# Performance work log

Hardware: AMD Instinct MI355X
Metric: run time of the kernel (lower is better)

## Reference

```python
import jax, jax.numpy as jnp
import numpy as np

T_STEPS, B, NMUL = 365, 20000, 4
NEARZERO = 1e-06

_BOUNDS = {
    'parBETA': (1.0, 6.0), 'parFC': (50.0, 1000.0), 'parK0': (0.05, 0.9),
    'parK1': (0.01, 0.5), 'parK2': (0.001, 0.2), 'parLP': (0.2, 1.0),
    'parPERC': (0.0, 10.0), 'parUZL': (0.0, 100.0), 'parTT': (-2.5, 2.5),
    'parCFMAX': (0.5, 10.0), 'parCFR': (0.0, 0.1), 'parCWH': (0.0, 0.2),
    'parBETAET': (0.3, 5.0), 'parC': (0.0, 1.0),
}


def setup_inputs() -> dict:
    key = jax.random.key(0)
    kf, kt, kp, *pkeys = jax.random.split(key, 3 + len(_BOUNDS))
    # forcing (T, B, 3): [prcp (mm/d), tmean (degC), pet (mm/d)]
    prcp = jax.random.uniform(kf, (T_STEPS, B), jnp.float32) * 10.0
    tmean = jax.random.normal(kt, (T_STEPS, B), jnp.float32) * 10.0
    pet = jax.random.uniform(kp, (T_STEPS, B), jnp.float32) * 5.0
    inp = {'forcing': jnp.stack([prcp, tmean, pet], axis=-1)}
    for k_rng, (name, (lo, hi)) in zip(pkeys, _BOUNDS.items()):
        inp[name] = jax.random.uniform(k_rng, (B, NMUL), jnp.float32, lo, hi)
    return inp


def _hbv_scan(forcing, parTT, parCFMAX, parCFR, parCWH, parFC, parBETA, parLP,
              parBETAET, parC, parPERC, parK0, parK1, parK2, parUZL):
    eps = NEARZERO
    nmul = parTT.shape[-1]
    n_grid = forcing.shape[1]
    # expand forcing to (T, B, nmul)
    Pm = jnp.broadcast_to(forcing[:, :, 0:1], forcing.shape[:2] + (nmul,))
    Tm = jnp.broadcast_to(forcing[:, :, 1:2], forcing.shape[:2] + (nmul,))
    PETm = jnp.broadcast_to(forcing[:, :, 2:3], forcing.shape[:2] + (nmul,))

    snow0 = jnp.full((n_grid, nmul), eps, forcing.dtype)
    zeros = jnp.zeros((n_grid, nmul), forcing.dtype)

    def step(carry, x):
        snow, melt, sm, suz, slz = carry
        p, t_val, pet = x
        temp_diff = t_val - parTT
        is_rain = temp_diff > 0.0
        rain = jnp.where(is_rain, p, 0.0)
        snow_input = jnp.where(is_rain, 0.0, p)
        snow1 = snow + snow_input
        pot_melt = parCFMAX * jnp.maximum(temp_diff, 0.0)
        melt_amount = jnp.minimum(pot_melt, snow1)
        snow2 = snow1 - melt_amount
        melt1 = melt + melt_amount
        pot_refreeze = parCFR * parCFMAX * jnp.maximum(-temp_diff, 0.0)
        refreeze = jnp.minimum(pot_refreeze, melt1)
        snow_out = snow2 + refreeze
        melt2 = melt1 - refreeze
        tosoil = jnp.maximum(melt2 - parCWH * snow_out, 0.0)
        melt_out = melt2 - tosoil
        soil_wet = jnp.clip(jnp.power(jnp.maximum(sm / parFC, eps), parBETA), 0.0, 1.0)
        recharge = (rain + tosoil) * soil_wet
        sm1 = sm + rain + tosoil - recharge
        excess = jnp.maximum(sm1 - parFC, 0.0)
        sm2 = sm1 - excess
        ef1 = jnp.clip(sm2 / (parLP * parFC), 0.0, 1.0)
        evapfactor = jnp.clip(jnp.power(jnp.maximum(ef1, eps), parBETAET), 0.0, 1.0)
        etact = jnp.minimum(pet * evapfactor, sm2)
        sm_ae = jnp.maximum(sm2 - etact, eps)
        sm_ratio = jnp.minimum(sm_ae / parFC, 1.0)
        capillary = jnp.minimum(slz, parC * slz * (1.0 - sm_ratio))
        sm_out = jnp.maximum(sm_ae + capillary, eps)
        slz_ac = jnp.maximum(slz - capillary, eps)
        suz1 = suz + recharge + excess
        perc_flux = jnp.minimum(suz1, parPERC)
        suz2 = suz1 - perc_flux
        slz1 = slz_ac + perc_flux
        q0 = parK0 * jnp.maximum(suz2 - parUZL, 0.0)
        suz3 = suz2 - q0
        q1 = parK1 * suz3
        suz_out = suz3 - q1
        q2 = parK2 * slz1
        slz_out = slz1 - q2
        q = q0 + q1 + q2
        return (snow_out, melt_out, sm_out, suz_out, slz_out), q

    _, Qsim = jax.lax.scan(step, (snow0, zeros, zeros, zeros, zeros), (Pm, Tm, PETm))
    return Qsim  # (T, B, nmul)


def reference(forcing, parTT, parCFMAX, parCFR, parCWH, parFC, parBETA, parLP,
              parBETAET, parC, parPERC, parK0, parK1, parK2, parUZL):
    Qsim = _hbv_scan(forcing, parTT, parCFMAX, parCFR, parCWH, parFC, parBETA,
                     parLP, parBETAET, parC, parPERC, parK0, parK1, parK2, parUZL)
    Qsim_avg = Qsim.mean(axis=-1)  # 'streamflow' (T, B)
    return (Qsim_avg, Qsim)
```

## Files before the change

### kernel.cpp

```cpp
#include <hip/hip_runtime.h>

#define TSTEPS 365
#define BGRID  20000
#define NMUL   4
#define NEARZERO 1e-6f
#define C    8
#define V    2
#define NCH  (TSTEPS / C)
#define TAIL (TSTEPS - NCH * C)

struct F3 { float p, t, pet; };

__device__ __forceinline__ float pair_swap(float x) {
    int a = __builtin_amdgcn_update_dpp(0, __float_as_int(x),
                                        0xB1 , 0xF, 0xF, true);
    return __int_as_float(a);
}

__device__ __forceinline__ float fast_log2(float x) { return __builtin_amdgcn_logf(x); }
__device__ __forceinline__ float fast_exp2(float x) { return __builtin_amdgcn_exp2f(x); }

#define LOAD_CHUNK(BUF, N)                                                  \
    _Pragma("unroll")                                                       \
    for (int j_ = 0; j_ < (N); ++j_) { BUF[j_] = *fp; fp += BGRID; }

#define STORE_CHUNK(QS, N)                                                  \
    _Pragma("unroll")                                                       \
    for (int j_ = 0; j_ < (N); ++j_) {                                      \
        qq[0] = QS[j_][0]; qq[2] = QS[j_][1]; qq += BGRID * NMUL;           \
        const float h_ = QS[j_][0] + QS[j_][1];                             \
        *qa = (h_ + pair_swap(h_)) * 0.25f; qa += BGRID;                    \
    }

#define COMPUTE_CHUNK(BUF, QO, N)                                           \
    _Pragma("unroll")                                                       \
    for (int j_ = 0; j_ < (N); ++j_) { step(BUF[j_], QO[j_]); }

__global__ __launch_bounds__(64) __attribute__((amdgpu_waves_per_eu(1, 2)))
void hbv_fwd(
    const float* __restrict__ forcing,
    const float* __restrict__ pBETA,  const float* __restrict__ pFC,
    const float* __restrict__ pK0,    const float* __restrict__ pK1,
    const float* __restrict__ pK2,    const float* __restrict__ pLP,
    const float* __restrict__ pPERC,  const float* __restrict__ pUZL,
    const float* __restrict__ pTT,    const float* __restrict__ pCFMAX,
    const float* __restrict__ pCFR,   const float* __restrict__ pCWH,
    const float* __restrict__ pBETAET,const float* __restrict__ pC,
    float* __restrict__ out_avg,
    float* __restrict__ out_q)
{
    const int tid = blockIdx.x * 64 + threadIdx.x;
    const int b  = tid >> 1;
    const int c0 = (b << 2) + (tid & 1);

    float parBETA[V], parFC[V], parK0[V], parK1[V], parK2[V], parPERC[V],
          parUZL[V], parTT[V], parCFMAX[V], parCWH[V], parBETAET[V], parC[V],
          refreeze_coef[V], inv_FC[V], inv_LPFC[V];
#pragma unroll
    for (int v = 0; v < V; ++v) {
        const int c = c0 + 2 * v;
        parBETA[v]   = pBETA[c];   parFC[v]   = pFC[c];
        parK0[v]     = pK0[c];     parK1[v]   = pK1[c];
        parK2[v]     = pK2[c];     parPERC[v] = pPERC[c];
        parUZL[v]    = pUZL[c];    parTT[v]   = pTT[c];
        parCFMAX[v]  = pCFMAX[c];  parCWH[v]  = pCWH[c];
        parBETAET[v] = pBETAET[c]; parC[v]    = pC[c];
        refreeze_coef[v] = pCFR[c] * parCFMAX[v];
        inv_FC[v]   = 1.0f / parFC[v];
        inv_LPFC[v] = 1.0f / (pLP[c] * parFC[v]);
    }

    float snow[V], melt[V], sm[V], suz[V], slz[V];
#pragma unroll
    for (int v = 0; v < V; ++v) {
        snow[v] = NEARZERO; melt[v] = 0.0f; sm[v] = 0.0f; suz[v] = 0.0f; slz[v] = 0.0f;
    }

    const F3* __restrict__ fp = (const F3*)forcing + b;
    float* __restrict__ qq = out_q + c0;
    float* __restrict__ qa = out_avg + b;

    auto step = [&](const F3 fv, float (&qo)[V]) {
#pragma unroll
        for (int v = 0; v < V; ++v) {
            const float temp_diff = fv.t - parTT[v];
            const bool  is_rain = temp_diff > 0.0f;
            const float rain       = is_rain ? fv.p : 0.0f;
            const float snow_input = is_rain ? 0.0f : fv.p;
            float snow1 = snow[v] + snow_input;
            const float pot_melt = parCFMAX[v] * fmaxf(temp_diff, 0.0f);
            const float melt_amount = fminf(pot_melt, snow1);
            snow1 -= melt_amount;
            float melt1 = melt[v] + melt_amount;
            const float pot_refreeze = refreeze_coef[v] * fmaxf(-temp_diff, 0.0f);
            const float refreeze = fminf(pot_refreeze, melt1);
            snow[v] = snow1 + refreeze;
            melt1 -= refreeze;
            const float tosoil = fmaxf(melt1 - parCWH[v] * snow[v], 0.0f);
            melt[v] = melt1 - tosoil;

            const float x1 = fmaxf(sm[v] * inv_FC[v], NEARZERO);
            const float soil_wet = fminf(fast_exp2(parBETA[v] * fast_log2(x1)), 1.0f);
            const float rt = rain + tosoil;
            const float recharge = rt * soil_wet;
            float sm1 = sm[v] + rt - recharge;
            const float excess = fmaxf(sm1 - parFC[v], 0.0f);
            sm1 -= excess;
            const float ef1 = fminf(sm1 * inv_LPFC[v], 1.0f);
            const float x2 = fmaxf(ef1, NEARZERO);
            const float evapfactor = fminf(fast_exp2(parBETAET[v] * fast_log2(x2)), 1.0f);
            const float etact = fminf(fv.pet * evapfactor, sm1);
            const float sm_ae = fmaxf(sm1 - etact, NEARZERO);
            const float sm_ratio = fminf(sm_ae * inv_FC[v], 1.0f);
            const float capillary = fminf(slz[v], parC[v] * slz[v] * (1.0f - sm_ratio));
            sm[v] = fmaxf(sm_ae + capillary, NEARZERO);
            float slz1 = fmaxf(slz[v] - capillary, NEARZERO);

            float suz1 = suz[v] + recharge + excess;
            const float perc_flux = fminf(suz1, parPERC[v]);
            suz1 -= perc_flux;
            slz1 += perc_flux;
            const float q0 = parK0[v] * fmaxf(suz1 - parUZL[v], 0.0f);
            suz1 -= q0;
            const float q1 = parK1[v] * suz1;
            suz[v] = suz1 - q1;
            const float q2 = parK2[v] * slz1;
            slz[v] = slz1 - q2;
            qo[v] = q0 + q1 + q2;
        }
    };

    F3 fA[C], fB[C];
    float qA[C][V], qB[C][V];

    LOAD_CHUNK(fA, C);

    LOAD_CHUNK(fB, C);
    COMPUTE_CHUNK(fA, qA, C);

#pragma clang loop unroll(disable)
    for (int p = 0; p < 21; ++p) {
        LOAD_CHUNK(fA, C);
        STORE_CHUNK(qA, C);
        COMPUTE_CHUNK(fB, qB, C);
        LOAD_CHUNK(fB, C);
        STORE_CHUNK(qB, C);
        COMPUTE_CHUNK(fA, qA, C);
    }
    LOAD_CHUNK(fA, C);
    STORE_CHUNK(qA, C);
    COMPUTE_CHUNK(fB, qB, C);
    LOAD_CHUNK(fB, TAIL);
    STORE_CHUNK(qB, C);
    COMPUTE_CHUNK(fA, qA, C);
    STORE_CHUNK(qA, C);
    COMPUTE_CHUNK(fB, qB, TAIL);
    STORE_CHUNK(qB, TAIL);
}

extern "C" void kernel_launch(void* const* d_in, const int* in_sizes, int n_in,
                              void* d_out, int out_size, void* d_ws, size_t ws_size,
                              hipStream_t stream) {
    const float* forcing = (const float*)d_in[0];

    float* out_avg = (float*)d_out;
    float* out_q   = out_avg + (size_t)TSTEPS * BGRID;

    const int total = BGRID * NMUL / V;
    const int block = 64;
    const int grid  = total / block;
    hbv_fwd<<<grid, block, 0, stream>>>(forcing,
        (const float*)d_in[1], (const float*)d_in[2], (const float*)d_in[3],
        (const float*)d_in[4], (const float*)d_in[5], (const float*)d_in[6],
        (const float*)d_in[7], (const float*)d_in[8], (const float*)d_in[9],
        (const float*)d_in[10], (const float*)d_in[11], (const float*)d_in[12],
        (const float*)d_in[13], (const float*)d_in[14],
        out_avg, out_q);
}
```

Baseline: 286.2 us.

## Process all four nmul members per thread with vectorized loads and stores

Each thread now handles one grid cell and all four NMUL members, instead of two threads each handling two members. The pair DPP swap goes away, and parameters and per-step outputs move with 16-byte vector loads and stores. The chunk size drops to 4 and the step arithmetic is tightened with fma and med3. The cost is half as many wavefronts, so latency hiding for the serial recurrence depends on the extra per-thread ILP from four independent chains.

Result: slower. 342.6 us (+19.7%).

```diff
diff --git a/kernel.cpp b/kernel.cpp
--- a/kernel.cpp
+++ b/kernel.cpp
@@ -4,21 +4,20 @@
 #define BGRID  20000
 #define NMUL   4
 #define NEARZERO 1e-6f
-#define C    8
-#define V    2
+#define C    4
 #define NCH  (TSTEPS / C)
 #define TAIL (TSTEPS - NCH * C)
+#define V    4
 
 struct F3 { float p, t, pet; };
-
-__device__ __forceinline__ float pair_swap(float x) {
-    int a = __builtin_amdgcn_update_dpp(0, __float_as_int(x),
-                                        0xB1 , 0xF, 0xF, true);
-    return __int_as_float(a);
-}
+typedef float f4v __attribute__((ext_vector_type(4)));
 
 __device__ __forceinline__ float fast_log2(float x) { return __builtin_amdgcn_logf(x); }
 __device__ __forceinline__ float fast_exp2(float x) { return __builtin_amdgcn_exp2f(x); }
+
+__device__ __forceinline__ f4v ld4(const float* p, int i) {
+    return *reinterpret_cast<const f4v*>(p + i);
+}
 
 #define LOAD_CHUNK(BUF, N)                                                  \
     _Pragma("unroll")                                                       \
@@ -27,16 +26,16 @@
 #define STORE_CHUNK(QS, N)                                                  \
     _Pragma("unroll")                                                       \
     for (int j_ = 0; j_ < (N); ++j_) {                                      \
-        qq[0] = QS[j_][0]; qq[2] = QS[j_][1]; qq += BGRID * NMUL;           \
-        const float h_ = QS[j_][0] + QS[j_][1];                             \
-        *qa = (h_ + pair_swap(h_)) * 0.25f; qa += BGRID;                    \
+        *qf = QS[j_]; qf += BGRID;         \
+        *qa = (((QS[j_].x + QS[j_].y) + (QS[j_].z + QS[j_].w))) * 0.25f;    \
+        qa += BGRID;                                                        \
     }
 
 #define COMPUTE_CHUNK(BUF, QO, N)                                           \
     _Pragma("unroll")                                                       \
     for (int j_ = 0; j_ < (N); ++j_) { step(BUF[j_], QO[j_]); }
 
-__global__ __launch_bounds__(64) __attribute__((amdgpu_waves_per_eu(1, 2)))
+__global__ __launch_bounds__(64) __attribute__((amdgpu_waves_per_eu(1, 1)))
 void hbv_fwd(
     const float* __restrict__ forcing,
     const float* __restrict__ pBETA,  const float* __restrict__ pFC,
@@ -49,25 +48,39 @@
     float* __restrict__ out_avg,
     float* __restrict__ out_q)
 {
-    const int tid = blockIdx.x * 64 + threadIdx.x;
-    const int b  = tid >> 1;
-    const int c0 = (b << 2) + (tid & 1);
+    const int b = blockIdx.x * 64 + threadIdx.x;
+    if (b >= BGRID) return;
+    const int c0 = b * 4;
+
+    const f4v vBETA   = ld4(pBETA, c0);
+    const f4v vFC     = ld4(pFC, c0);
+    const f4v vK0     = ld4(pK0, c0);
+    const f4v vK1     = ld4(pK1, c0);
+    const f4v vK2     = ld4(pK2, c0);
+    const f4v vLP     = ld4(pLP, c0);
+    const f4v vPERC   = ld4(pPERC, c0);
+    const f4v vUZL    = ld4(pUZL, c0);
+    const f4v vTT     = ld4(pTT, c0);
+    const f4v vCFMAX  = ld4(pCFMAX, c0);
+    const f4v vCFR    = ld4(pCFR, c0);
+    const f4v vCWH    = ld4(pCWH, c0);
+    const f4v vBETAET = ld4(pBETAET, c0);
+    const f4v vC      = ld4(pC, c0);
 
     float parBETA[V], parFC[V], parK0[V], parK1[V], parK2[V], parPERC[V],
           parUZL[V], parTT[V], parCFMAX[V], parCWH[V], parBETAET[V], parC[V],
           refreeze_coef[V], inv_FC[V], inv_LPFC[V];
 #pragma unroll
     for (int v = 0; v < V; ++v) {
-        const int c = c0 + 2 * v;
-        parBETA[v]   = pBETA[c];   parFC[v]   = pFC[c];
-        parK0[v]     = pK0[c];     parK1[v]   = pK1[c];
-        parK2[v]     = pK2[c];     parPERC[v] = pPERC[c];
-        parUZL[v]    = pUZL[c];    parTT[v]   = pTT[c];
-        parCFMAX[v]  = pCFMAX[c];  parCWH[v]  = pCWH[c];
-        parBETAET[v] = pBETAET[c]; parC[v]    = pC[c];
-        refreeze_coef[v] = pCFR[c] * parCFMAX[v];
+        parBETA[v]   = vBETA[v];   parFC[v]   = vFC[v];
+        parK0[v]     = vK0[v];     parK1[v]   = vK1[v];
+        parK2[v]     = vK2[v];     parPERC[v] = vPERC[v];
+        parUZL[v]    = vUZL[v];    parTT[v]   = vTT[v];
+        parCFMAX[v]  = vCFMAX[v];  parCWH[v]  = vCWH[v];
+        parBETAET[v] = vBETAET[v]; parC[v]    = vC[v];
+        refreeze_coef[v] = vCFR[v] * parCFMAX[v];
         inv_FC[v]   = 1.0f / parFC[v];
-        inv_LPFC[v] = 1.0f / (pLP[c] * parFC[v]);
+        inv_LPFC[v] = 1.0f / (vLP[v] * parFC[v]);
     }
 
     float snow[V], melt[V], sm[V], suz[V], slz[V];
@@ -77,69 +90,69 @@
     }
 
     const F3* __restrict__ fp = (const F3*)forcing + b;
-    float* __restrict__ qq = out_q + c0;
+    f4v* __restrict__ qf = (f4v*)(out_q + c0);
     float* __restrict__ qa = out_avg + b;
 
-    auto step = [&](const F3 fv, float (&qo)[V]) {
+    auto step = [&](const F3 fv, f4v &qo) {
+        float q[V];
 #pragma unroll
         for (int v = 0; v < V; ++v) {
-            const float temp_diff = fv.t - parTT[v];
-            const bool  is_rain = temp_diff > 0.0f;
-            const float rain       = is_rain ? fv.p : 0.0f;
-            const float snow_input = is_rain ? 0.0f : fv.p;
-            float snow1 = snow[v] + snow_input;
-            const float pot_melt = parCFMAX[v] * fmaxf(temp_diff, 0.0f);
-            const float melt_amount = fminf(pot_melt, snow1);
-            snow1 -= melt_amount;
-            float melt1 = melt[v] + melt_amount;
-            const float pot_refreeze = refreeze_coef[v] * fmaxf(-temp_diff, 0.0f);
-            const float refreeze = fminf(pot_refreeze, melt1);
-            snow[v] = snow1 + refreeze;
-            melt1 -= refreeze;
-            const float tosoil = fmaxf(melt1 - parCWH[v] * snow[v], 0.0f);
+            const float td = fv.t - parTT[v];
+            const float rain    = td > 0.0f ? fv.p : 0.0f;
+            const float snow_in = fv.p - rain;
+            float snow1 = snow[v] + snow_in;
+            const float pot_melt = parCFMAX[v] * fmaxf(td, 0.0f);
+            const float melt_amt = fminf(pot_melt, snow1);
+            snow1 -= melt_amt;
+            float melt1 = melt[v] + melt_amt;
+            const float pot_rfz = refreeze_coef[v] * fmaxf(-td, 0.0f);
+            const float rfz = fminf(pot_rfz, melt1);
+            snow[v] = snow1 + rfz;
+            melt1 -= rfz;
+            const float tosoil = fmaxf(fmaf(-parCWH[v], snow[v], melt1), 0.0f);
             melt[v] = melt1 - tosoil;
 
             const float x1 = fmaxf(sm[v] * inv_FC[v], NEARZERO);
             const float soil_wet = fminf(fast_exp2(parBETA[v] * fast_log2(x1)), 1.0f);
             const float rt = rain + tosoil;
             const float recharge = rt * soil_wet;
-            float sm1 = sm[v] + rt - recharge;
-            const float excess = fmaxf(sm1 - parFC[v], 0.0f);
-            sm1 -= excess;
-            const float ef1 = fminf(sm1 * inv_LPFC[v], 1.0f);
-            const float x2 = fmaxf(ef1, NEARZERO);
-            const float evapfactor = fminf(fast_exp2(parBETAET[v] * fast_log2(x2)), 1.0f);
-            const float etact = fminf(fv.pet * evapfactor, sm1);
-            const float sm_ae = fmaxf(sm1 - etact, NEARZERO);
-            const float sm_ratio = fminf(sm_ae * inv_FC[v], 1.0f);
-            const float capillary = fminf(slz[v], parC[v] * slz[v] * (1.0f - sm_ratio));
-            sm[v] = fmaxf(sm_ae + capillary, NEARZERO);
-            float slz1 = fmaxf(slz[v] - capillary, NEARZERO);
+            const float sm1 = (sm[v] + rt) - recharge;
+            const float sm2 = fminf(sm1, parFC[v]);
+            const float excess = sm1 - sm2;
+            const float x2 = __builtin_amdgcn_fmed3f(sm2 * inv_LPFC[v], NEARZERO, 1.0f);
+            const float ef = fminf(fast_exp2(parBETAET[v] * fast_log2(x2)), 1.0f);
+            const float sm_ae = fmaxf(fmaf(-fv.pet, ef, sm2), NEARZERO);
+            const float omr = fmaxf(fmaf(-inv_FC[v], sm_ae, 1.0f), 0.0f);
+            const float cslz = parC[v] * slz[v];
+            const float cap = fminf(slz[v], cslz * omr);
+            sm[v] = fmaxf(sm_ae + cap, NEARZERO);
+            const float slz_ac = fmaxf(slz[v] - cap, NEARZERO);
 
-            float suz1 = suz[v] + recharge + excess;
-            const float perc_flux = fminf(suz1, parPERC[v]);
-            suz1 -= perc_flux;
-            slz1 += perc_flux;
-            const float q0 = parK0[v] * fmaxf(suz1 - parUZL[v], 0.0f);
-            suz1 -= q0;
-            const float q1 = parK1[v] * suz1;
-            suz[v] = suz1 - q1;
+            const float suz1 = (suz[v] + recharge) + excess;
+            const float suz2 = fmaxf(suz1 - parPERC[v], 0.0f);
+            const float perc = suz1 - suz2;
+            const float slz1 = slz_ac + perc;
+            const float q0 = parK0[v] * fmaxf(suz2 - parUZL[v], 0.0f);
+            const float suz3 = suz2 - q0;
+            const float q1 = parK1[v] * suz3;
+            suz[v] = fmaf(-parK1[v], suz3, suz3);
             const float q2 = parK2[v] * slz1;
-            slz[v] = slz1 - q2;
-            qo[v] = q0 + q1 + q2;
+            slz[v] = fmaf(-parK2[v], slz1, slz1);
+            q[v] = (q0 + q1) + q2;
         }
+        f4v r; r.x = q[0]; r.y = q[1]; r.z = q[2]; r.w = q[3];
+        qo = r;
     };
 
     F3 fA[C], fB[C];
-    float qA[C][V], qB[C][V];
+    f4v qA[C], qB[C];
 
     LOAD_CHUNK(fA, C);
-
     LOAD_CHUNK(fB, C);
     COMPUTE_CHUNK(fA, qA, C);
 
 #pragma clang loop unroll(disable)
-    for (int p = 0; p < 21; ++p) {
+    for (int p = 0; p < 44; ++p) {
         LOAD_CHUNK(fA, C);
         STORE_CHUNK(qA, C);
         COMPUTE_CHUNK(fB, qB, C);
@@ -166,9 +179,9 @@
     float* out_avg = (float*)d_out;
     float* out_q   = out_avg + (size_t)TSTEPS * BGRID;
 
-    const int total = BGRID * NMUL / V;
+    const int total = BGRID;
     const int block = 64;
-    const int grid  = total / block;
+    const int grid  = (total + block - 1) / block;
     hbv_fwd<<<grid, block, 0, stream>>>(forcing,
         (const float*)d_in[1], (const float*)d_in[2], (const float*)d_in[3],
         (const float*)d_in[4], (const float*)d_in[5], (const float*)d_in[6],
```
